# Performance work log

Hardware: AMD Instinct MI355X
Metric: run time of the kernel (lower is better)

The kernel has to match this reference:

```python
import jax, jax.numpy as jnp
import numpy as np

# Eigenvalue spec: (alpha, omega, multiplicity); field='complex' => d_state = sum(mul)
EIGS = [(-0.4, 0.0, 32), (-0.3, 3.14, 32), (-0.2, 6.28, 32), (-0.1, 12.57, 32),
        (-0.05, 25.13, 32), (-0.02, 50.27, 32), (-0.01, 100.53, 32), (-0.005, 201.06, 32)]
DELTA_MIN, DELTA_MAX = 1e-3, 1e-1
B_SZ, H, L = 8, 128, 8192  # batch, d_input, seq length


def setup_inputs() -> dict:
    key = jax.random.key(0)
    k_delta, k_bre, k_bim, k_cre, k_cim, k_d, k_u = jax.random.split(key, 7)
    # continuous-time diagonal state matrix Lambda (P,) complex
    Lam = np.concatenate([np.full(m, a + 1j * w, dtype=np.complex64) for a, w, m in EIGS])
    Lambda = jnp.asarray(Lam)  # (P,)
    P = Lambda.shape[0]
    # ZOH discretization (done at init in the torch module)
    Delta = DELTA_MIN + (DELTA_MAX - DELTA_MIN) * jax.random.uniform(k_delta, (P,), dtype=jnp.float32)
    Lambda_bar = jnp.exp(Lambda * Delta)  # (P,) complex64
    B = (jax.random.normal(k_bre, (P, H), dtype=jnp.float32)
         + 1j * jax.random.normal(k_bim, (P, H), dtype=jnp.float32))
    B_bar = (((Lambda_bar - 1.0) / Lambda)[:, None] * B).astype(jnp.complex64)  # (P,H)
    C_re = jax.random.normal(k_cre, (H, P), dtype=jnp.float32)
    C_im = jax.random.normal(k_cim, (H, P), dtype=jnp.float32)
    D = jax.random.normal(k_d, (H, H), dtype=jnp.float32)
    u = jax.random.normal(k_u, (B_SZ, H, L), dtype=jnp.float32)
    return {
        "u": u,
        "Lambda_bar_re": jnp.real(Lambda_bar), "Lambda_bar_im": jnp.imag(Lambda_bar),
        "B_bar_re": jnp.real(B_bar), "B_bar_im": jnp.imag(B_bar),
        "C_re": C_re, "C_im": C_im, "D": D,
    }


def reference(u, Lambda_bar_re, Lambda_bar_im, B_bar_re, B_bar_im, C_re, C_im, D):
    Lambda_bar = Lambda_bar_re + 1j * Lambda_bar_im          # (P,)
    B_bar = B_bar_re + 1j * B_bar_im                         # (P,H)
    C = C_re + 1j * C_im                                     # (H,P)
    uc = u.astype(B_bar.dtype)
    Bu = jnp.einsum('ph,bhl->bpl', B_bar, uc)                # (B,P,L) complex
    A = jnp.broadcast_to(Lambda_bar[None, :, None], Bu.shape)  # (B,P,L)
    # The repo's binary op computes the sequential recurrence x_t = A_t * (x_{t-1} + Bu_t).
    # Rewriting with Bu'_t = A_t * Bu_t gives x_t = A_t x_{t-1} + Bu'_t, which is the
    # standard (truly associative) first-order scan.
    ABu = A * Bu

    def binop(ei, ej):
        a_i, b_i = ei
        a_j, b_j = ej
        return a_j * a_i, a_j * b_i + b_j

    _, xs = jax.lax.associative_scan(binop, (A, ABu), axis=2)  # xs: (B,P,L)
    y = jnp.einsum('op,bpl->bol', C, xs).real + jnp.einsum('oh,bhl->bol', D, u)
    return jax.nn.gelu(y, approximate=False)  # torch nn.GELU default = exact erf
```

## Files before the change

### kernel.cpp

```cpp
#include <hip/hip_runtime.h>
#include <math.h>

#define Bn 8
#define Hd 128
#define Ld 8192
#define Pd 256
#define LC 32
#define NC 256

typedef __attribute__((ext_vector_type(8))) short bf16x8;
typedef __attribute__((ext_vector_type(4))) float f32x4;
#define MFMA16(a, b, c) __builtin_amdgcn_mfma_f32_16x16x32_bf16(a, b, c, 0, 0, 0)

__device__ __forceinline__ unsigned short f2bf(float f) {
  unsigned u = __float_as_uint(f);
  u = u + 0x7fffu + ((u >> 16) & 1u);
  return (unsigned short)(u >> 16);
}

#if __has_builtin(__builtin_amdgcn_cvt_pk_bf16_f32)
typedef __attribute__((ext_vector_type(2))) __bf16 v2bf_t;
__device__ __forceinline__ unsigned pack2(float a, float b) {
  v2bf_t r = __builtin_amdgcn_cvt_pk_bf16_f32(a, b);
  unsigned u;
  __builtin_memcpy(&u, &r, 4);
  return u;
}
#else
__device__ __forceinline__ unsigned pack2(float a, float b) {
  return (unsigned)f2bf(a) | ((unsigned)f2bf(b) << 16);
}
#endif

__device__ __forceinline__ float bflo(unsigned v) { return __uint_as_float(v << 16); }
__device__ __forceinline__ float bfhi(unsigned v) { return __uint_as_float(v & 0xffff0000u); }

__device__ __forceinline__ int bperm(int p) {
  return ((p & 4) << 2) | ((p & 16) >> 1) | ((p & 8) >> 1) | (p & 3);
}

__global__ void k_prep(const float* __restrict__ Bre, const float* __restrict__ Bim,
                       const float* __restrict__ Cre, const float* __restrict__ Cim,
                       const float* __restrict__ Dm,
                       bf16x8* __restrict__ Bfr, bf16x8* __restrict__ Bfi,
                       bf16x8* __restrict__ Cf, bf16x8* __restrict__ Df) {
  int tid = blockIdx.x * 256 + threadIdx.x;
  int lane = tid & 63, slot = tid >> 6;
  int q = lane >> 4, ln = lane & 15;
  if (slot < 64) {
    int ks = slot >> 4, mt = slot & 15;
    int p = mt * 16 + ln;
    bf16x8 vr, vi;
#pragma unroll
    for (int e = 0; e < 8; ++e) {
      int h = ks * 32 + q * 8 + e;
      vr[e] = (short)f2bf(Bre[p * Hd + h]);
      vi[e] = (short)f2bf(Bim[p * Hd + h]);
    }
    Bfr[slot * 64 + lane] = vr;
    Bfi[slot * 64 + lane] = vi;
  } else if (slot < 64 + 128) {
    int s2 = slot - 64;
    int ks = s2 >> 3, mt = s2 & 7;
    int o = mt * 16 + ln;
    bf16x8 v;
#pragma unroll
    for (int e = 0; e < 8; ++e) {
      int kp = ks * 32 + q * 8 + e;
      int p = kp >> 1;
      float val = (kp & 1) ? -Cim[o * Pd + p] : Cre[o * Pd + p];
      v[e] = (short)f2bf(val);
    }
    Cf[s2 * 64 + lane] = v;
  } else if (slot < 64 + 128 + 32) {
    int s3 = slot - 192;
    int ks = s3 >> 3, mt = s3 & 7;
    int o = mt * 16 + ln;
    bf16x8 v;
#pragma unroll
    for (int e = 0; e < 8; ++e) {
      int h = ks * 32 + q * 8 + e;
      v[e] = (short)f2bf(Dm[o * Hd + h]);
    }
    Df[s3 * 64 + lane] = v;
  }
}

__device__ __forceinline__ void stage_u(const float* __restrict__ ub, unsigned* us32, int t) {
  int lane = t & 63, w = t >> 6;
  int j0 = 4 * (lane & 7);
  int h2 = 16 * w + 2 * (lane >> 3);
  const float* r0 = ub + (size_t)h2 * Ld + j0;
  float4 a0 = *(const float4*)r0;
  float4 a1 = *(const float4*)(r0 + Ld);
  const float* r2 = r0 + (size_t)64 * Ld;
  float4 b0 = *(const float4*)r2;
  float4 b1 = *(const float4*)(r2 + Ld);
  float ta0[4] = {a0.x, a0.y, a0.z, a0.w};
  float ta1[4] = {a1.x, a1.y, a1.z, a1.w};
  float tb0[4] = {b0.x, b0.y, b0.z, b0.w};
  float tb1[4] = {b1.x, b1.y, b1.z, b1.w};
#pragma unroll
  for (int i = 0; i < 4; ++i) {
    int j = j0 + i;
    int g1 = (h2 >> 3) ^ (j & 7);
    us32[(j * 256 + (g1 << 4) + ((2 * h2) & 15)) >> 2] = pack2(ta0[i], ta1[i]);
    int hb = h2 + 64;
    int g2 = (hb >> 3) ^ (j & 7);
    us32[(j * 256 + (g2 << 4) + ((2 * hb) & 15)) >> 2] = pack2(tb0[i], tb1[i]);
  }
}

__device__ __forceinline__ void compute_bu(const unsigned* us32,
                                           const bf16x8* __restrict__ Bfr,
                                           const bf16x8* __restrict__ Bfi,
                                           unsigned* bu32, int t) {
  int lane = t & 63, w = t >> 6, q = lane >> 4, ln = lane & 15;
  f32x4 zz = {0.f, 0.f, 0.f, 0.f};
  f32x4 aR[4][2], aI[4][2];
#pragma unroll
  for (int mt = 0; mt < 4; ++mt)
#pragma unroll
    for (int n = 0; n < 2; ++n) { aR[mt][n] = zz; aI[mt][n] = zz; }

#pragma unroll
  for (int ks = 0; ks < 4; ++ks) {
    bf16x8 ubf[2];
#pragma unroll
    for (int n = 0; n < 2; ++n) {
      int j = 16 * n + ln;
      int g = (4 * ks + q) ^ (j & 7);
      ubf[n] = *(const bf16x8*)((const char*)us32 + j * 256 + g * 16);
    }
#pragma unroll
    for (int mt = 0; mt < 4; ++mt) {
      int tI = ks * 16 + w * 4 + mt;
      bf16x8 ar = Bfr[tI * 64 + lane];
      bf16x8 ai = Bfi[tI * 64 + lane];
#pragma unroll
      for (int n = 0; n < 2; ++n) {
        aR[mt][n] = MFMA16(ar, ubf[n], aR[mt][n]);
        aI[mt][n] = MFMA16(ai, ubf[n], aI[mt][n]);
      }
    }
  }
#pragma unroll
  for (int mt = 0; mt < 4; ++mt)
#pragma unroll
    for (int n = 0; n < 2; ++n)
#pragma unroll
      for (int r = 0; r < 4; ++r) {
        int p = w * 64 + mt * 16 + q * 4 + r;
        int j = 16 * n + ln;
        bu32[(p << 5) | (j ^ bperm(p))] = pack2(aR[mt][n][r], aI[mt][n][r]);
      }
}

__global__ __launch_bounds__(256, 4) void k_chunkP(
    const float* __restrict__ u, const float* __restrict__ lre,
    const float* __restrict__ lim, const bf16x8* __restrict__ Bfr,
    const bf16x8* __restrict__ Bfi, const bf16x8* __restrict__ Cf,
    const bf16x8* __restrict__ Df, float2* __restrict__ E,
    float* __restrict__ p0out) {
  int bc = blockIdx.x;
  int b = bc >> 8, c = bc & 255;
  __shared__ __align__(16) unsigned char smem[8192 + 32768];
  unsigned* us32 = (unsigned*)smem;
  unsigned* bu32 = (unsigned*)(smem + 8192);
  unsigned* xs32 = bu32;
  int t = threadIdx.x;
  int lane = t & 63, w = t >> 6, q = lane >> 4, ln = lane & 15;

  stage_u(u + (size_t)b * Hd * Ld + c * LC, us32, t);
  __syncthreads();
  compute_bu(us32, Bfr, Bfi, bu32, t);
  __syncthreads();

  int p = t;
  int pm = bperm(p);
  unsigned v[LC];
#pragma unroll
  for (int j = 0; j < LC; ++j) v[j] = bu32[(p << 5) | (j ^ pm)];
  __syncthreads();

  {
    float ax = lre[p], ay = lim[p];
    float xr = 0.f, xi = 0.f;
#pragma unroll
    for (int j = 0; j < LC; ++j) {
      float sr = xr + bflo(v[j]), si = xi + bfhi(v[j]);
      xr = ax * sr - ay * si;
      xi = ax * si + ay * sr;
      xs32[j * 256 + ((((p >> 2) ^ (j & 7)) << 2) + (p & 3))] = pack2(xr, xi);
    }
    E[(size_t)bc * Pd + p] = make_float2(xr, xi);
  }
  __syncthreads();

  f32x4 zz = {0.f, 0.f, 0.f, 0.f};
  f32x4 acc[2][2] = {{zz, zz}, {zz, zz}};
#pragma unroll
  for (int ks = 0; ks < 16; ++ks) {
    bf16x8 xb[2];
#pragma unroll
    for (int n = 0; n < 2; ++n) {
      int j = 16 * n + ln;
      int g = (4 * ks + q) ^ (j & 7);
      xb[n] = *(const bf16x8*)((const char*)xs32 + j * 1024 + g * 16);
    }
#pragma unroll
    for (int mt = 0; mt < 2; ++mt) {
      bf16x8 cf = Cf[(ks * 8 + w * 2 + mt) * 64 + lane];
#pragma unroll
      for (int n = 0; n < 2; ++n) acc[mt][n] = MFMA16(cf, xb[n], acc[mt][n]);
    }
  }
#pragma unroll
  for (int ks = 0; ks < 4; ++ks) {
    bf16x8 ubf[2];
#pragma unroll
    for (int n = 0; n < 2; ++n) {
      int j = 16 * n + ln;
      int g = (4 * ks + q) ^ (j & 7);
      ubf[n] = *(const bf16x8*)((const char*)us32 + j * 256 + g * 16);
    }
#pragma unroll
    for (int mt = 0; mt < 2; ++mt) {
      bf16x8 df = Df[(ks * 8 + w * 2 + mt) * 64 + lane];
#pragma unroll
      for (int n = 0; n < 2; ++n) acc[mt][n] = MFMA16(df, ubf[n], acc[mt][n]);
    }
  }
#pragma unroll
  for (int mt = 0; mt < 2; ++mt)
#pragma unroll
    for (int n = 0; n < 2; ++n)
#pragma unroll
      for (int r = 0; r < 4; ++r) {
        int o = w * 32 + mt * 16 + q * 4 + r;
        p0out[((size_t)bc * Hd + o) * LC + 16 * n + ln] = acc[mt][n][r];
      }
}

__global__ __launch_bounds__(256) void k_scan(const float* __restrict__ lre,
                                              const float* __restrict__ lim,
                                              float2* __restrict__ E) {
  __shared__ float2 arr[32][8];
  int nb = blockIdx.x;
  int t = threadIdx.x;
  int pl = t & 7, rq = t >> 3;
  int b = nb >> 5;
  int p = ((nb & 31) << 3) + pl;
  float ax = lre[p], ay = lim[p];
  float mx = ax, my = ay;
#pragma unroll
  for (int k = 0; k < 5; ++k) {
    float nx = mx * mx - my * my, ny = 2.f * mx * my;
    mx = nx; my = ny;
  }
  size_t base = ((size_t)(b * NC + rq * 8)) * Pd + p;
  float2 pre[8];
  float cr = 0.f, ci = 0.f;
#pragma unroll
  for (int i = 0; i < 8; ++i) {
    float2 e = E[base + (size_t)i * Pd];
    pre[i] = make_float2(cr, ci);
    float nx = mx * cr - my * ci + e.x;
    float ny = mx * ci + my * cr + e.y;
    cr = nx; ci = ny;
  }
  float Mx = mx, My = my;
#pragma unroll
  for (int k = 0; k < 3; ++k) {
    float nx = Mx * Mx - My * My, ny = 2.f * Mx * My;
    Mx = nx; My = ny;
  }
  float Vx = cr, Vy = ci;
#pragma unroll
  for (int d = 1; d < 32; d <<= 1) {
    arr[rq][pl] = make_float2(Vx, Vy);
    __syncthreads();
    if (rq >= d) {
      float2 pv = arr[rq - d][pl];
      Vx += Mx * pv.x - My * pv.y;
      Vy += Mx * pv.y + My * pv.x;
    }
    __syncthreads();
    float nx = Mx * Mx - My * My, ny = 2.f * Mx * My;
    Mx = nx; My = ny;
  }
  arr[rq][pl] = make_float2(Vx, Vy);
  __syncthreads();
  float Cx = 0.f, Cy = 0.f;
  if (rq > 0) {
    float2 pv = arr[rq - 1][pl];
    Cx = pv.x; Cy = pv.y;
  }
  float tx = 1.f, ty = 0.f;
#pragma unroll
  for (int i = 0; i < 8; ++i) {
    float ox = pre[i].x + tx * Cx - ty * Cy;
    float oy = pre[i].y + tx * Cy + ty * Cx;
    E[base + (size_t)i * Pd] = make_float2(ox, oy);
    float nx = tx * mx - ty * my, ny = tx * my + ty * mx;
    tx = nx; ty = ny;
  }
}

__global__ __launch_bounds__(256, 4) void k_main2(
    const float* __restrict__ lre, const float* __restrict__ lim,
    const bf16x8* __restrict__ Cf, const float2* __restrict__ E,
    const float* __restrict__ p0in, float* __restrict__ out) {
  int bc = blockIdx.x;
  int b = bc >> 8, c = bc & 255;
  __shared__ __align__(16) unsigned xs32[LC * 256];
  int t = threadIdx.x;
  int lane = t & 63, w = t >> 6, q = lane >> 4, ln = lane & 15;

  float p0[16];
#pragma unroll
  for (int mt = 0; mt < 2; ++mt)
#pragma unroll
    for (int n = 0; n < 2; ++n)
#pragma unroll
      for (int r = 0; r < 4; ++r) {
        int o = w * 32 + mt * 16 + q * 4 + r;
        p0[mt * 8 + n * 4 + r] = p0in[((size_t)bc * Hd + o) * LC + 16 * n + ln];
      }

  int p = t;
  float2 xin = E[(size_t)bc * Pd + p];
  float ax = lre[p], ay = lim[p];
  float gr = ax * xin.x - ay * xin.y;
  float gi = ax * xin.y + ay * xin.x;
#pragma unroll
  for (int j = 0; j < LC; ++j) {
    xs32[j * 256 + ((((p >> 2) ^ (j & 7)) << 2) + (p & 3))] = pack2(gr, gi);
    float nr = ax * gr - ay * gi, ni = ax * gi + ay * gr;
    gr = nr; gi = ni;
  }
  __syncthreads();

  f32x4 zz = {0.f, 0.f, 0.f, 0.f};
  f32x4 acc[2][2] = {{zz, zz}, {zz, zz}};
#pragma unroll
  for (int ks = 0; ks < 16; ++ks) {
    bf16x8 xb[2];
#pragma unroll
    for (int n = 0; n < 2; ++n) {
      int j = 16 * n + ln;
      int g = (4 * ks + q) ^ (j & 7);
      xb[n] = *(const bf16x8*)((const char*)xs32 + j * 1024 + g * 16);
    }
#pragma unroll
    for (int mt = 0; mt < 2; ++mt) {
      bf16x8 cf = Cf[(ks * 8 + w * 2 + mt) * 64 + lane];
#pragma unroll
      for (int n = 0; n < 2; ++n) acc[mt][n] = MFMA16(cf, xb[n], acc[mt][n]);
    }
  }

#pragma unroll
  for (int mt = 0; mt < 2; ++mt)
#pragma unroll
    for (int n = 0; n < 2; ++n)
#pragma unroll
      for (int r = 0; r < 4; ++r) {
        int o = w * 32 + mt * 16 + q * 4 + r;
        int l = c * LC + 16 * n + ln;
        float vy = acc[mt][n][r] + p0[mt * 8 + n * 4 + r];
        float e2 = __builtin_amdgcn_exp2f(-2.4554670f * vy);
        float gy = vy * __builtin_amdgcn_rcpf(1.0f + e2);
        out[((size_t)(b * Hd + o)) * Ld + l] = gy;
      }
}

extern "C" void kernel_launch(void* const* d_in, const int* in_sizes, int n_in,
                              void* d_out, int out_size, void* d_ws, size_t ws_size,
                              hipStream_t stream) {
  const float* u   = (const float*)d_in[0];
  const float* lre = (const float*)d_in[1];
  const float* lim = (const float*)d_in[2];
  const float* Bre = (const float*)d_in[3];
  const float* Bim = (const float*)d_in[4];
  const float* Cre = (const float*)d_in[5];
  const float* Cim = (const float*)d_in[6];
  const float* Dm  = (const float*)d_in[7];
  float* out = (float*)d_out;

  char* ws = (char*)d_ws;
  bf16x8* Bfr = (bf16x8*)(ws);
  bf16x8* Bfi = (bf16x8*)(ws + 65536);
  bf16x8* Cf  = (bf16x8*)(ws + 131072);
  bf16x8* Df  = (bf16x8*)(ws + 262144);
  float2* E   = (float2*)(ws + (1u << 20));
  float*  P0  = (float*)(ws + (16u << 20));

  k_prep<<<56, 256, 0, stream>>>(Bre, Bim, Cre, Cim, Dm, Bfr, Bfi, Cf, Df);
  k_chunkP<<<Bn * NC, 256, 0, stream>>>(u, lre, lim, Bfr, Bfi, Cf, Df, E, P0);
  k_scan<<<256, 256, 0, stream>>>(lre, lim, E);
  k_main2<<<Bn * NC, 256, 0, stream>>>(lre, lim, Cf, E, P0, out);
}
```

Baseline: 148.4 us.

## Process two chunks per block with prefetch, bf16 partial outputs, split-step correction fill

Each block in k_chunkP and k_main2 now handles two consecutive chunks, halving the grid. The second chunk's u tile is loaded into registers while the first chunk computes. The intermediate projection P0 is stored as packed bf16 pairs instead of fp32, halving its write and read traffic. The correction fill runs two independent power chains using Lambda^2 to shorten the serial dependency. The risks are lower parallelism (1024 blocks), more register pressure from the prefetched data, and added bf16 rounding on P0.

```diff
diff --git a/kernel.cpp b/kernel.cpp
--- a/kernel.cpp
+++ b/kernel.cpp
@@ -86,20 +86,30 @@
   }
 }
 
-__device__ __forceinline__ void stage_u(const float* __restrict__ ub, unsigned* us32, int t) {
+struct ust { float4 a0, a1, b0, b1; };
+
+__device__ __forceinline__ ust stage_load(const float* __restrict__ ub, int t) {
   int lane = t & 63, w = t >> 6;
   int j0 = 4 * (lane & 7);
   int h2 = 16 * w + 2 * (lane >> 3);
   const float* r0 = ub + (size_t)h2 * Ld + j0;
-  float4 a0 = *(const float4*)r0;
-  float4 a1 = *(const float4*)(r0 + Ld);
+  ust s;
+  s.a0 = *(const float4*)r0;
+  s.a1 = *(const float4*)(r0 + Ld);
   const float* r2 = r0 + (size_t)64 * Ld;
-  float4 b0 = *(const float4*)r2;
-  float4 b1 = *(const float4*)(r2 + Ld);
-  float ta0[4] = {a0.x, a0.y, a0.z, a0.w};
-  float ta1[4] = {a1.x, a1.y, a1.z, a1.w};
-  float tb0[4] = {b0.x, b0.y, b0.z, b0.w};
-  float tb1[4] = {b1.x, b1.y, b1.z, b1.w};
+  s.b0 = *(const float4*)r2;
+  s.b1 = *(const float4*)(r2 + Ld);
+  return s;
+}
+
+__device__ __forceinline__ void stage_write(const ust& s, unsigned* us32, int t) {
+  int lane = t & 63, w = t >> 6;
+  int j0 = 4 * (lane & 7);
+  int h2 = 16 * w + 2 * (lane >> 3);
+  float ta0[4] = {s.a0.x, s.a0.y, s.a0.z, s.a0.w};
+  float ta1[4] = {s.a1.x, s.a1.y, s.a1.z, s.a1.w};
+  float tb0[4] = {s.b0.x, s.b0.y, s.b0.z, s.b0.w};
+  float tb1[4] = {s.b1.x, s.b1.y, s.b1.z, s.b1.w};
 #pragma unroll
   for (int i = 0; i < 4; ++i) {
     int j = j0 + i;
@@ -156,90 +166,112 @@
       }
 }
 
+__device__ __forceinline__ void capture_v(const unsigned* bu32, unsigned (&v)[LC],
+                                          int p, int pm) {
+#pragma unroll
+  for (int j = 0; j < LC; ++j) v[j] = bu32[(p << 5) | (j ^ pm)];
+}
+
+__device__ __forceinline__ void scan_chunk(unsigned* xs32, float2* __restrict__ E,
+                                           const unsigned (&v)[LC], int bc, int p,
+                                           float ax, float ay) {
+  float xr = 0.f, xi = 0.f;
+#pragma unroll
+  for (int j = 0; j < LC; ++j) {
+    float sr = xr + bflo(v[j]), si = xi + bfhi(v[j]);
+    xr = ax * sr - ay * si;
+    xi = ax * si + ay * sr;
+    xs32[j * 256 + ((((p >> 2) ^ (j & 7)) << 2) + (p & 3))] = pack2(xr, xi);
+  }
+  E[(size_t)bc * Pd + p] = make_float2(xr, xi);
+}
+
+__device__ __forceinline__ void projectP(const bf16x8* __restrict__ Cf,
+                                         const bf16x8* __restrict__ Df,
+                                         const unsigned* us32, const unsigned* xs32,
+                                         unsigned* __restrict__ p0out, int bc, int t) {
+  int lane = t & 63, w = t >> 6, q = lane >> 4, ln = lane & 15;
+  f32x4 zz = {0.f, 0.f, 0.f, 0.f};
+  f32x4 acc[2][2] = {{zz, zz}, {zz, zz}};
+#pragma unroll
+  for (int ks = 0; ks < 16; ++ks) {
+    bf16x8 xb[2];
+#pragma unroll
+    for (int n = 0; n < 2; ++n) {
+      int j = 16 * n + ln;
+      int g = (4 * ks + q) ^ (j & 7);
+      xb[n] = *(const bf16x8*)((const char*)xs32 + j * 1024 + g * 16);
+    }
+#pragma unroll
+    for (int mt = 0; mt < 2; ++mt) {
+      bf16x8 cf = Cf[(ks * 8 + w * 2 + mt) * 64 + lane];
+#pragma unroll
+      for (int n = 0; n < 2; ++n) acc[mt][n] = MFMA16(cf, xb[n], acc[mt][n]);
+    }
+  }
+#pragma unroll
+  for (int ks = 0; ks < 4; ++ks) {
+    bf16x8 ubf[2];
+#pragma unroll
+    for (int n = 0; n < 2; ++n) {
+      int j = 16 * n + ln;
+      int g = (4 * ks + q) ^ (j & 7);
+      ubf[n] = *(const bf16x8*)((const char*)us32 + j * 256 + g * 16);
+    }
+#pragma unroll
+    for (int mt = 0; mt < 2; ++mt) {
+      bf16x8 df = Df[(ks * 8 + w * 2 + mt) * 64 + lane];
+#pragma unroll
+      for (int n = 0; n < 2; ++n) acc[mt][n] = MFMA16(df, ubf[n], acc[mt][n]);
+    }
+  }
+#pragma unroll
+  for (int mt = 0; mt < 2; ++mt)
+#pragma unroll
+    for (int r = 0; r < 4; ++r) {
+      int o = w * 32 + mt * 16 + q * 4 + r;
+      p0out[(size_t)bc * 2048 + o * 16 + ln] = pack2(acc[mt][0][r], acc[mt][1][r]);
+    }
+}
+
 __global__ __launch_bounds__(256, 4) void k_chunkP(
     const float* __restrict__ u, const float* __restrict__ lre,
     const float* __restrict__ lim, const bf16x8* __restrict__ Bfr,
     const bf16x8* __restrict__ Bfi, const bf16x8* __restrict__ Cf,
     const bf16x8* __restrict__ Df, float2* __restrict__ E,
-    float* __restrict__ p0out) {
-  int bc = blockIdx.x;
-  int b = bc >> 8, c = bc & 255;
+    unsigned* __restrict__ p0out) {
+  int blk = blockIdx.x;
+  int b = blk >> 7;
+  int cA = (blk & 127) * 2;
+  int bcA = (b << 8) | cA;
   __shared__ __align__(16) unsigned char smem[8192 + 32768];
   unsigned* us32 = (unsigned*)smem;
   unsigned* bu32 = (unsigned*)(smem + 8192);
-  unsigned* xs32 = bu32;
   int t = threadIdx.x;
-  int lane = t & 63, w = t >> 6, q = lane >> 4, ln = lane & 15;
-
-  stage_u(u + (size_t)b * Hd * Ld + c * LC, us32, t);
-  __syncthreads();
+  int p = t, pm = bperm(p);
+  float ax = lre[p], ay = lim[p];
+  const float* ubase = u + (size_t)b * Hd * Ld;
+
+  ust sA = stage_load(ubase + cA * LC, t);
+  stage_write(sA, us32, t);
+  __syncthreads();
+  ust sB = stage_load(ubase + cA * LC + LC, t);
   compute_bu(us32, Bfr, Bfi, bu32, t);
-  __syncthreads();
-
-  int p = t;
-  int pm = bperm(p);
   unsigned v[LC];
-#pragma unroll
-  for (int j = 0; j < LC; ++j) v[j] = bu32[(p << 5) | (j ^ pm)];
-  __syncthreads();
-
-  {
-    float ax = lre[p], ay = lim[p];
-    float xr = 0.f, xi = 0.f;
-#pragma unroll
-    for (int j = 0; j < LC; ++j) {
-      float sr = xr + bflo(v[j]), si = xi + bfhi(v[j]);
-      xr = ax * sr - ay * si;
-      xi = ax * si + ay * sr;
-      xs32[j * 256 + ((((p >> 2) ^ (j & 7)) << 2) + (p & 3))] = pack2(xr, xi);
-    }
-    E[(size_t)bc * Pd + p] = make_float2(xr, xi);
-  }
-  __syncthreads();
-
-  f32x4 zz = {0.f, 0.f, 0.f, 0.f};
-  f32x4 acc[2][2] = {{zz, zz}, {zz, zz}};
-#pragma unroll
-  for (int ks = 0; ks < 16; ++ks) {
-    bf16x8 xb[2];
-#pragma unroll
-    for (int n = 0; n < 2; ++n) {
-      int j = 16 * n + ln;
-      int g = (4 * ks + q) ^ (j & 7);
-      xb[n] = *(const bf16x8*)((const char*)xs32 + j * 1024 + g * 16);
-    }
-#pragma unroll
-    for (int mt = 0; mt < 2; ++mt) {
-      bf16x8 cf = Cf[(ks * 8 + w * 2 + mt) * 64 + lane];
-#pragma unroll
-      for (int n = 0; n < 2; ++n) acc[mt][n] = MFMA16(cf, xb[n], acc[mt][n]);
-    }
-  }
-#pragma unroll
-  for (int ks = 0; ks < 4; ++ks) {
-    bf16x8 ubf[2];
-#pragma unroll
-    for (int n = 0; n < 2; ++n) {
-      int j = 16 * n + ln;
-      int g = (4 * ks + q) ^ (j & 7);
-      ubf[n] = *(const bf16x8*)((const char*)us32 + j * 256 + g * 16);
-    }
-#pragma unroll
-    for (int mt = 0; mt < 2; ++mt) {
-      bf16x8 df = Df[(ks * 8 + w * 2 + mt) * 64 + lane];
-#pragma unroll
-      for (int n = 0; n < 2; ++n) acc[mt][n] = MFMA16(df, ubf[n], acc[mt][n]);
-    }
-  }
-#pragma unroll
-  for (int mt = 0; mt < 2; ++mt)
-#pragma unroll
-    for (int n = 0; n < 2; ++n)
-#pragma unroll
-      for (int r = 0; r < 4; ++r) {
-        int o = w * 32 + mt * 16 + q * 4 + r;
-        p0out[((size_t)bc * Hd + o) * LC + 16 * n + ln] = acc[mt][n][r];
-      }
+  capture_v(bu32, v, p, pm);
+  __syncthreads();
+  scan_chunk(bu32, E, v, bcA, p, ax, ay);
+  __syncthreads();
+  projectP(Cf, Df, us32, bu32, p0out, bcA, t);
+  __syncthreads();
+  stage_write(sB, us32, t);
+  __syncthreads();
+  compute_bu(us32, Bfr, Bfi, bu32, t);
+  capture_v(bu32, v, p, pm);
+  __syncthreads();
+  scan_chunk(bu32, E, v, bcA + 1, p, ax, ay);
+  __syncthreads();
+  projectP(Cf, Df, us32, bu32, p0out, bcA + 1, t);
 }
 
 __global__ __launch_bounds__(256) void k_scan(const float* __restrict__ lre,
@@ -307,40 +339,27 @@
   }
 }
 
-__global__ __launch_bounds__(256, 4) void k_main2(
-    const float* __restrict__ lre, const float* __restrict__ lim,
-    const bf16x8* __restrict__ Cf, const float2* __restrict__ E,
-    const float* __restrict__ p0in, float* __restrict__ out) {
-  int bc = blockIdx.x;
-  int b = bc >> 8, c = bc & 255;
-  __shared__ __align__(16) unsigned xs32[LC * 256];
-  int t = threadIdx.x;
+__device__ __forceinline__ void corr_fill(unsigned* xs32, float2 xin, float ax,
+                                          float ay, float a2r, float a2i, int p) {
+  float g0r = ax * xin.x - ay * xin.y, g0i = ax * xin.y + ay * xin.x;
+  float g1r = a2r * xin.x - a2i * xin.y, g1i = a2r * xin.y + a2i * xin.x;
+#pragma unroll
+  for (int j = 0; j < LC; j += 2) {
+    xs32[j * 256 + ((((p >> 2) ^ (j & 7)) << 2) + (p & 3))] = pack2(g0r, g0i);
+    int j1 = j + 1;
+    xs32[j1 * 256 + ((((p >> 2) ^ (j1 & 7)) << 2) + (p & 3))] = pack2(g1r, g1i);
+    float n0r = a2r * g0r - a2i * g0i, n0i = a2r * g0i + a2i * g0r;
+    float n1r = a2r * g1r - a2i * g1i, n1i = a2r * g1i + a2i * g1r;
+    g0r = n0r; g0i = n0i; g1r = n1r; g1i = n1i;
+  }
+}
+
+__device__ __forceinline__ void proj_corr_store(const bf16x8* __restrict__ Cf,
+                                                const unsigned* xs32,
+                                                const unsigned (&p0)[8],
+                                                float* __restrict__ out, int b,
+                                                int c, int t) {
   int lane = t & 63, w = t >> 6, q = lane >> 4, ln = lane & 15;
-
-  float p0[16];
-#pragma unroll
-  for (int mt = 0; mt < 2; ++mt)
-#pragma unroll
-    for (int n = 0; n < 2; ++n)
-#pragma unroll
-      for (int r = 0; r < 4; ++r) {
-        int o = w * 32 + mt * 16 + q * 4 + r;
-        p0[mt * 8 + n * 4 + r] = p0in[((size_t)bc * Hd + o) * LC + 16 * n + ln];
-      }
-
-  int p = t;
-  float2 xin = E[(size_t)bc * Pd + p];
-  float ax = lre[p], ay = lim[p];
-  float gr = ax * xin.x - ay * xin.y;
-  float gi = ax * xin.y + ay * xin.x;
-#pragma unroll
-  for (int j = 0; j < LC; ++j) {
-    xs32[j * 256 + ((((p >> 2) ^ (j & 7)) << 2) + (p & 3))] = pack2(gr, gi);
-    float nr = ax * gr - ay * gi, ni = ax * gi + ay * gr;
-    gr = nr; gi = ni;
-  }
-  __syncthreads();
-
   f32x4 zz = {0.f, 0.f, 0.f, 0.f};
   f32x4 acc[2][2] = {{zz, zz}, {zz, zz}};
 #pragma unroll
@@ -359,7 +378,6 @@
       for (int n = 0; n < 2; ++n) acc[mt][n] = MFMA16(cf, xb[n], acc[mt][n]);
     }
   }
-
 #pragma unroll
   for (int mt = 0; mt < 2; ++mt)
 #pragma unroll
@@ -368,11 +386,48 @@
       for (int r = 0; r < 4; ++r) {
         int o = w * 32 + mt * 16 + q * 4 + r;
         int l = c * LC + 16 * n + ln;
-        float vy = acc[mt][n][r] + p0[mt * 8 + n * 4 + r];
+        float pv = n ? bfhi(p0[mt * 4 + r]) : bflo(p0[mt * 4 + r]);
+        float vy = acc[mt][n][r] + pv;
         float e2 = __builtin_amdgcn_exp2f(-2.4554670f * vy);
         float gy = vy * __builtin_amdgcn_rcpf(1.0f + e2);
         out[((size_t)(b * Hd + o)) * Ld + l] = gy;
       }
+}
+
+__global__ __launch_bounds__(256, 4) void k_main2(
+    const float* __restrict__ lre, const float* __restrict__ lim,
+    const bf16x8* __restrict__ Cf, const float2* __restrict__ E,
+    const unsigned* __restrict__ p0in, float* __restrict__ out) {
+  int blk = blockIdx.x;
+  int b = blk >> 7;
+  int cA = (blk & 127) * 2;
+  int bcA = (b << 8) | cA;
+  __shared__ __align__(16) unsigned xs32[LC * 256];
+  int t = threadIdx.x;
+  int lane = t & 63, w = t >> 6, q = lane >> 4, ln = lane & 15;
+  int p = t;
+  float ax = lre[p], ay = lim[p];
+  float a2r = ax * ax - ay * ay, a2i = 2.f * ax * ay;
+
+  unsigned pA[8], pB[8];
+#pragma unroll
+  for (int mt = 0; mt < 2; ++mt)
+#pragma unroll
+    for (int r = 0; r < 4; ++r) {
+      int o = w * 32 + mt * 16 + q * 4 + r;
+      pA[mt * 4 + r] = p0in[(size_t)bcA * 2048 + o * 16 + ln];
+      pB[mt * 4 + r] = p0in[(size_t)(bcA + 1) * 2048 + o * 16 + ln];
+    }
+  float2 xinA = E[(size_t)bcA * Pd + p];
+  float2 xinB = E[(size_t)(bcA + 1) * Pd + p];
+
+  corr_fill(xs32, xinA, ax, ay, a2r, a2i, p);
+  __syncthreads();
+  proj_corr_store(Cf, xs32, pA, out, b, cA, t);
+  __syncthreads();
+  corr_fill(xs32, xinB, ax, ay, a2r, a2i, p);
+  __syncthreads();
+  proj_corr_store(Cf, xs32, pB, out, b, cA + 1, t);
 }
 
 extern "C" void kernel_launch(void* const* d_in, const int* in_sizes, int n_in,
@@ -394,10 +449,10 @@
   bf16x8* Cf  = (bf16x8*)(ws + 131072);
   bf16x8* Df  = (bf16x8*)(ws + 262144);
   float2* E   = (float2*)(ws + (1u << 20));
-  float*  P0  = (float*)(ws + (16u << 20));
+  unsigned* P0 = (unsigned*)(ws + (16u << 20));
 
   k_prep<<<56, 256, 0, stream>>>(Bre, Bim, Cre, Cim, Dm, Bfr, Bfi, Cf, Df);
-  k_chunkP<<<Bn * NC, 256, 0, stream>>>(u, lre, lim, Bfr, Bfi, Cf, Df, E, P0);
+  k_chunkP<<<1024, 256, 0, stream>>>(u, lre, lim, Bfr, Bfi, Cf, Df, E, P0);
   k_scan<<<256, 256, 0, stream>>>(lre, lim, E);
-  k_main2<<<Bn * NC, 256, 0, stream>>>(lre, lim, Cf, E, P0, out);
-}
+  k_main2<<<1024, 256, 0, stream>>>(lre, lim, Cf, E, P0, out);
+}
```

Result: slower. 187.2 us (+26.1%).
